# Kernel tuning notes

Measured on AMD Instinct MI355X. Metric: run time of the kernel, lower is better.

The kernel has to match this reference:

```python
import jax, jax.numpy as jnp
import numpy as np

STATE_DIM = 512
PROJ_DIM = 300


def setup_inputs() -> dict:
    key = jax.random.key(0)
    ks = jax.random.split(key, 10)
    batseq, node_num, edge_num = 320, 32, 1024  # edge_num = node_num**2
    inp = {
        "nodes_feats": jax.random.normal(ks[0], (batseq, node_num, STATE_DIM), jnp.float32),
        "edges_feats": jax.random.normal(ks[1], (batseq, edge_num, STATE_DIM), jnp.float32),
        "adj_mat": jax.random.uniform(ks[2], (batseq, node_num, edge_num), jnp.float32),
        "true_lengths": jax.random.randint(ks[3], (32,), 0, 10),
        "seq_size": 10,
        # Linear layer params (out_features=300, in_features=512), torch layout W: [out, in]
        "W1": jax.random.normal(ks[4], (PROJ_DIM, STATE_DIM), jnp.float32) * 0.02,
        "b1": jnp.zeros((PROJ_DIM,), jnp.float32),
        "W2": jax.random.normal(ks[5], (PROJ_DIM, STATE_DIM), jnp.float32) * 0.02,
        "b2": jnp.zeros((PROJ_DIM,), jnp.float32),
        "W3": jax.random.normal(ks[6], (PROJ_DIM, STATE_DIM), jnp.float32) * 0.02,
        "b3": jnp.zeros((PROJ_DIM,), jnp.float32),
    }
    return inp


def reference(nodes_feats, edges_feats, adj_mat, true_lengths, seq_size,
              W1, b1, W2, b2, W3, b3):
    batseq, node_num, _ = nodes_feats.shape
    batch = batseq // seq_size  # from adj_mat.view(-1, seq_size, node_num, edge_num)
    # Batched replacements for the per-pair tiny Linears
    f1 = jnp.einsum("bnd,pd->bnp", nodes_feats, W1) + b1   # [B, N, 300]
    f3 = jnp.einsum("bnd,pd->bnp", nodes_feats, W3) + b3   # [B, N, 300]
    f2 = jnp.einsum("bed,pd->bep", edges_feats, W2) + b2   # [B, N*N, 300]
    f2 = f2.reshape(batseq, node_num, node_num, PROJ_DIM)  # [B, i, j, 300]
    # per-pair MSE(f_j, f_ij + f_i), mean over (batseq, 300), summed over (i, j)
    diff = f3[:, None, :, :] - f2 - f1[:, :, None, :]
    losses = jnp.sum(diff * diff) / (batseq * PROJ_DIM)
    return losses / batch
```

## Files before the change

kernel.cpp:

```cpp
#include <hip/hip_runtime.h>
#include <hip/hip_bf16.h>
#include <stdint.h>

#define STATE 512
#define PROJ 300
#define PPAD 320
#define BATSEQ 320
#define TE 327680
#define PSTR 328

typedef __bf16 bf16x8 __attribute__((ext_vector_type(8)));
typedef float f32x4 __attribute__((ext_vector_type(4)));
typedef float f32x2 __attribute__((ext_vector_type(2)));
typedef long long i64;

__device__ inline unsigned short f2bf(float x) {
  unsigned u = __builtin_bit_cast(unsigned, x);
  unsigned r = u + 0x7fffu + ((u >> 16) & 1u);
  return (unsigned short)(r >> 16);
}

__global__ __launch_bounds__(256) void prep_kernel(
    const float* __restrict__ W1, const float* __restrict__ b1,
    const float* __restrict__ W2, const float* __restrict__ b2,
    const float* __restrict__ W3, const float* __restrict__ b3,
    unsigned short* __restrict__ w1p, unsigned short* __restrict__ w3p,
    unsigned short* __restrict__ w2tp, unsigned char* __restrict__ w2p8,
    float* __restrict__ b1p, float* __restrict__ b2p, float* __restrict__ b3p)
{
  int idx = blockIdx.x * 256 + threadIdx.x;
  const int WN = PPAD * STATE;
  if (idx < 2 * WN) {
    int which = idx / WN, r = idx % WN;
    int cs = r / 512, q = r % 512;
    int lane = q / 8, i = q % 8;
    int c = cs / 16, s = cs % 16;
    int p = c * 16 + (lane & 15);
    int k = s * 32 + (lane >> 4) * 8 + i;
    const float* W = (which == 0) ? W1 : W3;
    unsigned short* dst = (which == 0) ? w1p : w3p;
    float v = (p < PROJ) ? W[(size_t)p * STATE + k] : 0.0f;
    dst[r] = f2bf(v);
  } else if (idx < 3 * WN) {
    int r = idx - 2 * WN;
    int cs = r / 512, q = r % 512;
    int lane = q / 8, ii = q % 8;
    int ct = cs / 10, s2 = cs % 10;
    int p = s2 * 32 + (lane >> 4) * 8 + ii;
    int n = ct * 16 + (lane & 15);
    float v = (p < PROJ) ? W2[(size_t)p * STATE + n] : 0.0f;
    w2tp[r] = f2bf(v);
  } else if (idx < 4 * WN) {
    int r = idx - 3 * WN;
    int cs = r / 512, q = r % 512;
    int lane = q / 8, i = q % 8;
    int c = cs / 16, s = cs % 16;
    int p = c * 16 + (lane & 15);
    int k = s * 32 + (lane >> 4) * 8 + i;
    float v = (p < PROJ) ? W2[(size_t)p * STATE + k] : 0.0f;
    int pk = __builtin_amdgcn_cvt_pk_fp8_f32(v, 0.f, 0, 0);
    w2p8[r] = (unsigned char)(pk & 0xff);
  } else if (idx < 4 * WN + 3 * PPAD) {
    int r = idx - 4 * WN;
    int which = r / PPAD, p = r % PPAD;
    const float* B = (which == 0) ? b1 : ((which == 1) ? b2 : b3);
    float* dst = (which == 0) ? b1p : ((which == 1) ? b2p : b3p);
    dst[p] = (p < PROJ) ? B[p] : 0.0f;
  }
}

__global__ __launch_bounds__(256, 2) void node_kernel(
    const float* __restrict__ nodes,
    const unsigned short* __restrict__ w1p, const unsigned short* __restrict__ w3p,
    const unsigned short* __restrict__ w2tp,
    const float* __restrict__ b1p, const float* __restrict__ b2p,
    const float* __restrict__ b3p,
    float* __restrict__ g1t, float* __restrict__ g3t,
    double* __restrict__ pnode)
{
  __shared__ __align__(16) unsigned short tile[32 * 512];
  __shared__ __align__(16) unsigned short t2a[32 * PSTR];
  __shared__ __align__(16) unsigned short t2b[32 * PSTR];
  __shared__ float G1[PPAD], G3[PPAD];
  __shared__ double red[4];
  const int tid = threadIdx.x;
  const int wave = tid >> 6, lane = tid & 63;
  const int b = blockIdx.x;
  const float* src = nodes + (size_t)b * 32 * STATE;

  for (int t = tid; t < PPAD; t += 256) { G1[t] = 0.f; G3[t] = 0.f; }

  #pragma unroll
  for (int m = 0; m < 16; ++m) {
    int k = wave + 4 * m;
    int row = k >> 1;
    int fc = (k & 1) * 64 + lane;
    f32x4 v = *(const f32x4*)(src + row * STATE + fc * 4);
    unsigned lo = f2bf(v.x) | ((unsigned)f2bf(v.y) << 16);
    unsigned hi = f2bf(v.z) | ((unsigned)f2bf(v.w) << 16);
    unsigned long long pk = (unsigned long long)lo | ((unsigned long long)hi << 32);
    unsigned off = (unsigned)(row * 1024 + fc * 8) ^ (unsigned)((row & 7) << 4);
    *(unsigned long long*)((char*)tile + off) = pk;
  }
  __syncthreads();

  const int lrow = lane & 15, lk = lane >> 4;
  const int cbase = wave * 5;

  f32x4 af1[2][5], af3[2][5];
  #pragma unroll
  for (int rg = 0; rg < 2; ++rg)
    #pragma unroll
    for (int c = 0; c < 5; ++c) {
      af1[rg][c][0]=0.f; af1[rg][c][1]=0.f; af1[rg][c][2]=0.f; af1[rg][c][3]=0.f;
      af3[rg][c][0]=0.f; af3[rg][c][1]=0.f; af3[rg][c][2]=0.f; af3[rg][c][3]=0.f;
    }
  for (int s = 0; s < 16; ++s) {
    bf16x8 a[2];
    #pragma unroll
    for (int rg = 0; rg < 2; ++rg) {
      int row = rg * 16 + lrow;
      unsigned off = (unsigned)(row * 1024 + s * 64 + lk * 16) ^ (unsigned)((row & 7) << 4);
      a[rg] = *(const bf16x8*)((const char*)tile + off);
    }
    #pragma unroll
    for (int c = 0; c < 5; ++c) {
      size_t fo = ((size_t)(((cbase + c) * 16 + s) * 64 + lane)) * 8;
      bf16x8 bf1 = *(const bf16x8*)(w1p + fo);
      bf16x8 bf3 = *(const bf16x8*)(w3p + fo);
      #pragma unroll
      for (int rg = 0; rg < 2; ++rg) {
        af1[rg][c] = __builtin_amdgcn_mfma_f32_16x16x32_bf16(a[rg], bf1, af1[rg][c], 0, 0, 0);
        af3[rg][c] = __builtin_amdgcn_mfma_f32_16x16x32_bf16(a[rg], bf3, af3[rg][c], 0, 0, 0);
      }
    }
  }

  float sq = 0.f;
  #pragma unroll
  for (int rg = 0; rg < 2; ++rg)
    #pragma unroll
    for (int c = 0; c < 5; ++c) {
      int p = (cbase + c) * 16 + lrow;
      float bb1 = b1p[p], bb2 = b2p[p], bb3 = b3p[p];
      #pragma unroll
      for (int r = 0; r < 4; ++r) {
        int m = rg * 16 + lk * 4 + r;
        float v1 = af1[rg][c][r] + bb1;
        float v3 = af3[rg][c][r] + bb3 - bb2;
        t2a[m * PSTR + p] = f2bf(v1);
        t2b[m * PSTR + p] = f2bf(v3);
        sq += v1 * v1 + v3 * v3;
        atomicAdd(&G1[p], v1);
        atomicAdd(&G3[p], v3);
      }
    }
  __syncthreads();

  float s7 = 0.f;
  for (int t = tid; t < PPAD; t += 256) s7 += G3[t] * G1[t];
  float val = 32.f * sq - 2.f * s7;
  #pragma unroll
  for (int m = 32; m >= 1; m >>= 1) val += __shfl_xor(val, m, 64);
  if (lane == 0) red[wave] = (double)val;

  for (int pass = 0; pass < 2; ++pass) {
    const unsigned short* t2 = pass ? t2b : t2a;
    float* gt = pass ? g3t : g1t;
    f32x4 acc2[2][8];
    #pragma unroll
    for (int rg = 0; rg < 2; ++rg)
      #pragma unroll
      for (int cc = 0; cc < 8; ++cc) { acc2[rg][cc][0]=0.f; acc2[rg][cc][1]=0.f; acc2[rg][cc][2]=0.f; acc2[rg][cc][3]=0.f; }
    for (int s2 = 0; s2 < 10; ++s2) {
      bf16x8 a[2];
      #pragma unroll
      for (int rg = 0; rg < 2; ++rg) {
        int mrow = rg * 16 + lrow;
        a[rg] = *(const bf16x8*)(t2 + mrow * PSTR + s2 * 32 + lk * 8);
      }
      #pragma unroll
      for (int cc = 0; cc < 8; ++cc) {
        int ct = wave * 8 + cc;
        bf16x8 bfr = *(const bf16x8*)(w2tp + ((size_t)((ct * 10 + s2) * 64 + lane)) * 8);
        #pragma unroll
        for (int rg = 0; rg < 2; ++rg)
          acc2[rg][cc] = __builtin_amdgcn_mfma_f32_16x16x32_bf16(a[rg], bfr, acc2[rg][cc], 0, 0, 0);
      }
    }
    #pragma unroll
    for (int rg = 0; rg < 2; ++rg)
      #pragma unroll
      for (int cc = 0; cc < 8; ++cc) {
        int n = (wave * 8 + cc) * 16 + lrow;
        #pragma unroll
        for (int r = 0; r < 4; ++r) {
          int mm = rg * 16 + lk * 4 + r;
          gt[((size_t)b * 32 + mm) * STATE + n] = acc2[rg][cc][r];
        }
      }
  }

  __syncthreads();
  if (tid == 0) pnode[b] = red[0] + red[1] + red[2] + red[3];
}

__global__ __launch_bounds__(256, 3) void edge_kernel(
    const float* __restrict__ edges, const unsigned char* __restrict__ w2p8,
    const float* __restrict__ g1t, const float* __restrict__ g3t,
    double* __restrict__ pedge)
{
  __shared__ __align__(16) unsigned char tile[64 * 512];
  __shared__ double redd[4][2];
  const int tid = threadIdx.x;
  const int wave = tid >> 6, lane = tid & 63;

  const int orig = blockIdx.x;
  const int wg = (orig & 7) * 640 + (orig >> 3);
  const int b = wg >> 4, q = wg & 15;
  const float* src = edges + ((size_t)b * 1024 + (size_t)q * 64) * STATE;
  const float* g3b = g3t + (size_t)b * 32 * STATE;
  const float* g1b = g1t + ((size_t)b * 32 + (size_t)q * 2) * STATE;

  float cr = 0.f;
  f32x4 sE0 = {0.f, 0.f, 0.f, 0.f}, sE1 = {0.f, 0.f, 0.f, 0.f};
  const int fc = tid & 127;
  const int rhi = tid >> 7;
  #pragma unroll 16
  for (int m = 0; m < 32; ++m) {
    int row = 2 * m + rhi;
    f32x4 e = *(const f32x4*)(src + row * STATE + fc * 4);
    if (m < 16) sE0 += e; else sE1 += e;
    int pk = __builtin_amdgcn_cvt_pk_fp8_f32(e.x, e.y, 0, 0);
    pk = __builtin_amdgcn_cvt_pk_fp8_f32(e.z, e.w, pk, 1);
    unsigned off = (unsigned)(row * 512 + fc * 4) ^ (unsigned)((row & 7) << 3);
    *(int*)(tile + off) = pk;
  }
  {
    f32x4 g1a = *(const f32x4*)(g1b + fc * 4);
    f32x4 g1c = *(const f32x4*)(g1b + STATE + fc * 4);
    cr -= sE0.x * g1a.x + sE0.y * g1a.y + sE0.z * g1a.z + sE0.w * g1a.w;
    cr -= sE1.x * g1c.x + sE1.y * g1c.y + sE1.z * g1c.z + sE1.w * g1c.w;
  }
  __syncthreads();

  const int lrow = lane & 15, lk = lane >> 4;
  const int cb = wave * 5;
  f32x4 acc[4][5];
  #pragma unroll
  for (int rg = 0; rg < 4; ++rg)
    #pragma unroll
    for (int c = 0; c < 5; ++c) { acc[rg][c][0]=0.f; acc[rg][c][1]=0.f; acc[rg][c][2]=0.f; acc[rg][c][3]=0.f; }
  for (int s = 0; s < 16; ++s) {
    i64 a[4];
    #pragma unroll
    for (int rg = 0; rg < 4; ++rg) {
      int row = rg * 16 + lrow;
      unsigned off = (unsigned)(row * 512 + s * 32 + lk * 8) ^ (unsigned)((row & 7) << 3);
      a[rg] = *(const i64*)(tile + off);
    }
    #pragma unroll
    for (int c = 0; c < 5; ++c) {
      i64 bfr = *(const i64*)(w2p8 + ((size_t)(((cb + c) * 16 + s) * 64 + lane)) * 8);
      #pragma unroll
      for (int rg = 0; rg < 4; ++rg)
        acc[rg][c] = __builtin_amdgcn_mfma_f32_16x16x32_fp8_fp8(a[rg], bfr, acc[rg][c], 0, 0, 0);
    }
  }

  float ss = 0.f;
  #pragma unroll
  for (int rg = 0; rg < 4; ++rg)
    #pragma unroll
    for (int c = 0; c < 5; ++c)
      #pragma unroll
      for (int r = 0; r < 4; ++r) ss += acc[rg][c][r] * acc[rg][c][r];

  {
    const int j = tid >> 3, s8 = tid & 7;
    const float* g3r = g3b + (size_t)j * STATE + s8 * 64;
    const unsigned sw = (unsigned)((j & 7) << 3);
    float part = 0.f;
    #pragma unroll
    for (int c = 0; c < 8; ++c) {
      unsigned o0 = (unsigned)(j * 512 + s8 * 64 + c * 8) ^ sw;
      unsigned o1 = (unsigned)((j + 32) * 512 + s8 * 64 + c * 8) ^ sw;
      i64 p0 = *(const i64*)(tile + o0);
      i64 p1 = *(const i64*)(tile + o1);
      int l0 = (int)(p0 & 0xffffffffll), h0 = (int)(((unsigned long long)p0) >> 32);
      int l1 = (int)(p1 & 0xffffffffll), h1 = (int)(((unsigned long long)p1) >> 32);
      f32x2 a0 = __builtin_amdgcn_cvt_pk_f32_fp8(l0, 0);
      f32x2 a1 = __builtin_amdgcn_cvt_pk_f32_fp8(l0, 1);
      f32x2 a2 = __builtin_amdgcn_cvt_pk_f32_fp8(h0, 0);
      f32x2 a3 = __builtin_amdgcn_cvt_pk_f32_fp8(h0, 1);
      f32x2 c0 = __builtin_amdgcn_cvt_pk_f32_fp8(l1, 0);
      f32x2 c1 = __builtin_amdgcn_cvt_pk_f32_fp8(l1, 1);
      f32x2 c2 = __builtin_amdgcn_cvt_pk_f32_fp8(h1, 0);
      f32x2 c3 = __builtin_amdgcn_cvt_pk_f32_fp8(h1, 1);
      f32x4 g0 = *(const f32x4*)(g3r + c * 8);
      f32x4 g1v = *(const f32x4*)(g3r + c * 8 + 4);
      part += (a0.x + c0.x) * g0.x + (a0.y + c0.y) * g0.y
            + (a1.x + c1.x) * g0.z + (a1.y + c1.y) * g0.w
            + (a2.x + c2.x) * g1v.x + (a2.y + c2.y) * g1v.y
            + (a3.x + c3.x) * g1v.z + (a3.y + c3.y) * g1v.w;
    }
    cr += part;
  }

  #pragma unroll
  for (int m = 32; m >= 1; m >>= 1) {
    ss += __shfl_xor(ss, m, 64);
    cr += __shfl_xor(cr, m, 64);
  }
  if (lane == 0) { redd[wave][0] = (double)ss; redd[wave][1] = (double)cr; }
  __syncthreads();
  if (tid == 0) {
    double sT = 0.0, cT = 0.0;
    #pragma unroll
    for (int w = 0; w < 4; ++w) { sT += redd[w][0]; cT += redd[w][1]; }
    pedge[wg] = sT - 2.0 * cT;
  }
}

__global__ __launch_bounds__(256) void final_kernel(
    const double* __restrict__ pedge, const double* __restrict__ pnode,
    const int* __restrict__ seqp, float* __restrict__ out)
{
  __shared__ double red[4];
  const int tid = threadIdx.x, wave = tid >> 6, lane = tid & 63;
  double v = 0.0;
  for (int t = tid; t < 5120; t += 256) v += pedge[t];
  for (int t = tid; t < 320; t += 256) v += pnode[t];
  #pragma unroll
  for (int m = 32; m >= 1; m >>= 1) v += __shfl_xor(v, m, 64);
  if (lane == 0) red[wave] = v;
  __syncthreads();
  if (tid == 0) {
    double Total = red[0] + red[1] + red[2] + red[3];
    int seq = seqp[0];
    int batch = (seq > 0) ? (BATSEQ / seq) : 1;
    out[0] = (float)(Total / ((double)BATSEQ * (double)PROJ) / (double)batch);
  }
}

extern "C" void kernel_launch(void* const* d_in, const int* in_sizes, int n_in,
                              void* d_out, int out_size, void* d_ws, size_t ws_size,
                              hipStream_t stream)
{
  const float* nodes = (const float*)d_in[0];
  const float* edges = (const float*)d_in[1];
  const int*   seqp  = (const int*)d_in[4];
  const float* W1 = (const float*)d_in[5];
  const float* b1 = (const float*)d_in[6];
  const float* W2 = (const float*)d_in[7];
  const float* b2 = (const float*)d_in[8];
  const float* W3 = (const float*)d_in[9];
  const float* b3 = (const float*)d_in[10];

  char* ws = (char*)d_ws;
  unsigned short* w1p  = (unsigned short*)(ws + 0);
  unsigned short* w3p  = (unsigned short*)(ws + 327680);
  unsigned short* w2tp = (unsigned short*)(ws + 655360);
  unsigned char*  w2p8 = (unsigned char*)(ws + 983040);
  float* b1p = (float*)(ws + 1146880);
  float* b2p = (float*)(ws + 1148160);
  float* b3p = (float*)(ws + 1149440);
  float* g1t = (float*)(ws + 2097152);
  float* g3t = (float*)(ws + 23068672);
  double* pedge = (double*)(ws + 44040192);
  double* pnode = (double*)(ws + 44081152);

  prep_kernel<<<2564, 256, 0, stream>>>(W1, b1, W2, b2, W3, b3,
                                        w1p, w3p, w2tp, w2p8, b1p, b2p, b3p);
  node_kernel<<<320, 256, 0, stream>>>(nodes, w1p, w3p, w2tp, b1p, b2p, b3p,
                                       g1t, g3t, pnode);
  edge_kernel<<<5120, 256, 0, stream>>>(edges, w2p8, g1t, g3t, pedge);
  final_kernel<<<1, 256, 0, stream>>>(pedge, pnode, seqp, (float*)d_out);
}
```

Baseline: 309.4 us.

## Double edge tile per block and compute g3 cross term with fp8 MFMA

Each edge block now handles 128 edge rows instead of 64, halving the grid and reusing each W2 fragment load across twice as many MFMAs. The scalar fp8-to-float dot product against g3 is replaced by extra MFMAs against a g3 matrix pre-packed to fp8 by a new small kernel, with only the diagonal entries kept. This trades higher register and LDS use, and lower occupancy (launch bounds drop to 2 blocks), for fewer global weight reads and less scalar ALU work. The g3 term now also runs at fp8 precision.

```diff
diff --git a/kernel.cpp b/kernel.cpp
--- a/kernel.cpp
+++ b/kernel.cpp
@@ -11,7 +11,6 @@
 
 typedef __bf16 bf16x8 __attribute__((ext_vector_type(8)));
 typedef float f32x4 __attribute__((ext_vector_type(4)));
-typedef float f32x2 __attribute__((ext_vector_type(2)));
 typedef long long i64;
 
 __device__ inline unsigned short f2bf(float x) {
@@ -205,106 +204,118 @@
   if (tid == 0) pnode[b] = red[0] + red[1] + red[2] + red[3];
 }
 
-__global__ __launch_bounds__(256, 3) void edge_kernel(
+__global__ __launch_bounds__(256) void g3pack_kernel(
+    const float* __restrict__ g3t, unsigned char* __restrict__ g3p8)
+{
+  const int b = blockIdx.x;
+  const float* g3b = g3t + (size_t)b * 32 * STATE;
+  int* dst = (int*)(g3p8 + (size_t)b * 16384);
+  #pragma unroll
+  for (int t = 0; t < 16; ++t) {
+    int g = threadIdx.x + t * 256;
+    int r = g * 4;
+    int lane = (r >> 3) & 63;
+    int i0 = r & 7;
+    int cts = r >> 9;
+    int j = (cts >> 4) * 16 + (lane & 15);
+    int k = (cts & 15) * 32 + (lane >> 4) * 8 + i0;
+    const float* v = g3b + (size_t)j * STATE + k;
+    int pk = __builtin_amdgcn_cvt_pk_fp8_f32(v[0], v[1], 0, 0);
+    pk = __builtin_amdgcn_cvt_pk_fp8_f32(v[2], v[3], pk, 1);
+    dst[g] = pk;
+  }
+}
+
+__global__ __launch_bounds__(256, 2) void edge_kernel(
     const float* __restrict__ edges, const unsigned char* __restrict__ w2p8,
-    const float* __restrict__ g1t, const float* __restrict__ g3t,
+    const unsigned char* __restrict__ g3p8, const float* __restrict__ g1t,
     double* __restrict__ pedge)
 {
-  __shared__ __align__(16) unsigned char tile[64 * 512];
+  __shared__ __align__(16) unsigned char tile[128 * 512];
   __shared__ double redd[4][2];
   const int tid = threadIdx.x;
   const int wave = tid >> 6, lane = tid & 63;
 
   const int orig = blockIdx.x;
-  const int wg = (orig & 7) * 640 + (orig >> 3);
-  const int b = wg >> 4, q = wg & 15;
-  const float* src = edges + ((size_t)b * 1024 + (size_t)q * 64) * STATE;
-  const float* g3b = g3t + (size_t)b * 32 * STATE;
-  const float* g1b = g1t + ((size_t)b * 32 + (size_t)q * 2) * STATE;
-
-  float cr = 0.f;
-  f32x4 sE0 = {0.f, 0.f, 0.f, 0.f}, sE1 = {0.f, 0.f, 0.f, 0.f};
+  const int wg = (orig & 7) * 320 + (orig >> 3);
+  const int b = wg >> 3, q4 = wg & 7;
+  const float* src = edges + ((size_t)b * 1024 + (size_t)q4 * 128) * STATE;
+  const unsigned char* g3p = g3p8 + (size_t)b * 16384;
+  const float* g1b = g1t + ((size_t)b * 32 + (size_t)q4 * 4) * STATE;
+
+  f32x4 sE[4];
+  #pragma unroll
+  for (int ii = 0; ii < 4; ++ii) { sE[ii][0]=0.f; sE[ii][1]=0.f; sE[ii][2]=0.f; sE[ii][3]=0.f; }
   const int fc = tid & 127;
   const int rhi = tid >> 7;
   #pragma unroll 16
-  for (int m = 0; m < 32; ++m) {
+  for (int m = 0; m < 64; ++m) {
     int row = 2 * m + rhi;
     f32x4 e = *(const f32x4*)(src + row * STATE + fc * 4);
-    if (m < 16) sE0 += e; else sE1 += e;
+    sE[m >> 4] += e;
     int pk = __builtin_amdgcn_cvt_pk_fp8_f32(e.x, e.y, 0, 0);
     pk = __builtin_amdgcn_cvt_pk_fp8_f32(e.z, e.w, pk, 1);
     unsigned off = (unsigned)(row * 512 + fc * 4) ^ (unsigned)((row & 7) << 3);
     *(int*)(tile + off) = pk;
   }
-  {
-    f32x4 g1a = *(const f32x4*)(g1b + fc * 4);
-    f32x4 g1c = *(const f32x4*)(g1b + STATE + fc * 4);
-    cr -= sE0.x * g1a.x + sE0.y * g1a.y + sE0.z * g1a.z + sE0.w * g1a.w;
-    cr -= sE1.x * g1c.x + sE1.y * g1c.y + sE1.z * g1c.z + sE1.w * g1c.w;
-  }
   __syncthreads();
 
   const int lrow = lane & 15, lk = lane >> 4;
   const int cb = wave * 5;
-  f32x4 acc[4][5];
-  #pragma unroll
-  for (int rg = 0; rg < 4; ++rg)
+  f32x4 acc[8][5];
+  #pragma unroll
+  for (int rg = 0; rg < 8; ++rg)
     #pragma unroll
     for (int c = 0; c < 5; ++c) { acc[rg][c][0]=0.f; acc[rg][c][1]=0.f; acc[rg][c][2]=0.f; acc[rg][c][3]=0.f; }
+  f32x4 accg[2];
+  accg[0][0]=0.f; accg[0][1]=0.f; accg[0][2]=0.f; accg[0][3]=0.f;
+  accg[1][0]=0.f; accg[1][1]=0.f; accg[1][2]=0.f; accg[1][3]=0.f;
+
+  #pragma unroll 4
   for (int s = 0; s < 16; ++s) {
-    i64 a[4];
-    #pragma unroll
-    for (int rg = 0; rg < 4; ++rg) {
+    i64 a[8];
+    #pragma unroll
+    for (int rg = 0; rg < 8; ++rg) {
       int row = rg * 16 + lrow;
-      unsigned off = (unsigned)(row * 512 + s * 32 + lk * 8) ^ (unsigned)((row & 7) << 3);
+      unsigned off = (unsigned)(row * 512 + s * 32 + lk * 8) ^ (unsigned)((lrow & 7) << 3);
       a[rg] = *(const i64*)(tile + off);
     }
+    i64 bg0 = *(const i64*)(g3p + ((size_t)((s) * 64 + lane)) * 8);
+    i64 bg1 = *(const i64*)(g3p + ((size_t)((16 + s) * 64 + lane)) * 8);
     #pragma unroll
     for (int c = 0; c < 5; ++c) {
       i64 bfr = *(const i64*)(w2p8 + ((size_t)(((cb + c) * 16 + s) * 64 + lane)) * 8);
       #pragma unroll
-      for (int rg = 0; rg < 4; ++rg)
+      for (int rg = 0; rg < 8; ++rg)
         acc[rg][c] = __builtin_amdgcn_mfma_f32_16x16x32_fp8_fp8(a[rg], bfr, acc[rg][c], 0, 0, 0);
     }
-  }
-
-  float ss = 0.f;
-  #pragma unroll
-  for (int rg = 0; rg < 4; ++rg)
+    #pragma unroll
+    for (int rg = 0; rg < 8; ++rg)
+      accg[rg & 1] = __builtin_amdgcn_mfma_f32_16x16x32_fp8_fp8(a[rg], (rg & 1) ? bg1 : bg0, accg[rg & 1], 0, 0, 0);
+  }
+
+  float ss = 0.f, cr = 0.f;
+  #pragma unroll
+  for (int rg = 0; rg < 8; ++rg)
     #pragma unroll
     for (int c = 0; c < 5; ++c)
       #pragma unroll
       for (int r = 0; r < 4; ++r) ss += acc[rg][c][r] * acc[rg][c][r];
 
   {
-    const int j = tid >> 3, s8 = tid & 7;
-    const float* g3r = g3b + (size_t)j * STATE + s8 * 64;
-    const unsigned sw = (unsigned)((j & 7) << 3);
-    float part = 0.f;
-    #pragma unroll
-    for (int c = 0; c < 8; ++c) {
-      unsigned o0 = (unsigned)(j * 512 + s8 * 64 + c * 8) ^ sw;
-      unsigned o1 = (unsigned)((j + 32) * 512 + s8 * 64 + c * 8) ^ sw;
-      i64 p0 = *(const i64*)(tile + o0);
-      i64 p1 = *(const i64*)(tile + o1);
-      int l0 = (int)(p0 & 0xffffffffll), h0 = (int)(((unsigned long long)p0) >> 32);
-      int l1 = (int)(p1 & 0xffffffffll), h1 = (int)(((unsigned long long)p1) >> 32);
-      f32x2 a0 = __builtin_amdgcn_cvt_pk_f32_fp8(l0, 0);
-      f32x2 a1 = __builtin_amdgcn_cvt_pk_f32_fp8(l0, 1);
-      f32x2 a2 = __builtin_amdgcn_cvt_pk_f32_fp8(h0, 0);
-      f32x2 a3 = __builtin_amdgcn_cvt_pk_f32_fp8(h0, 1);
-      f32x2 c0 = __builtin_amdgcn_cvt_pk_f32_fp8(l1, 0);
-      f32x2 c1 = __builtin_amdgcn_cvt_pk_f32_fp8(l1, 1);
-      f32x2 c2 = __builtin_amdgcn_cvt_pk_f32_fp8(h1, 0);
-      f32x2 c3 = __builtin_amdgcn_cvt_pk_f32_fp8(h1, 1);
-      f32x4 g0 = *(const f32x4*)(g3r + c * 8);
-      f32x4 g1v = *(const f32x4*)(g3r + c * 8 + 4);
-      part += (a0.x + c0.x) * g0.x + (a0.y + c0.y) * g0.y
-            + (a1.x + c1.x) * g0.z + (a1.y + c1.y) * g0.w
-            + (a2.x + c2.x) * g1v.x + (a2.y + c2.y) * g1v.y
-            + (a3.x + c3.x) * g1v.z + (a3.y + c3.y) * g1v.w;
-    }
-    cr += part;
+    int qv = lane & 15, hi4 = lane >> 4;
+    if ((qv >> 2) == hi4) {
+      int r = qv & 3;
+      float d0 = (r == 0) ? accg[0][0] : (r == 1) ? accg[0][1] : (r == 2) ? accg[0][2] : accg[0][3];
+      float d1 = (r == 0) ? accg[1][0] : (r == 1) ? accg[1][1] : (r == 2) ? accg[1][2] : accg[1][3];
+      cr += d0 + d1;
+    }
+  }
+
+  #pragma unroll
+  for (int ii = 0; ii < 4; ++ii) {
+    f32x4 g1v = *(const f32x4*)(g1b + (size_t)ii * STATE + fc * 4);
+    cr -= sE[ii].x * g1v.x + sE[ii].y * g1v.y + sE[ii].z * g1v.z + sE[ii].w * g1v.w;
   }
 
   #pragma unroll
@@ -329,7 +340,7 @@
   __shared__ double red[4];
   const int tid = threadIdx.x, wave = tid >> 6, lane = tid & 63;
   double v = 0.0;
-  for (int t = tid; t < 5120; t += 256) v += pedge[t];
+  for (int t = tid; t < 2560; t += 256) v += pedge[t];
   for (int t = tid; t < 320; t += 256) v += pnode[t];
   #pragma unroll
   for (int m = 32; m >= 1; m >>= 1) v += __shfl_xor(v, m, 64);
@@ -368,12 +379,14 @@
   float* g1t = (float*)(ws + 2097152);
   float* g3t = (float*)(ws + 23068672);
   double* pedge = (double*)(ws + 44040192);
-  double* pnode = (double*)(ws + 44081152);
+  double* pnode = (double*)(ws + 44060672);
+  unsigned char* g3p8 = (unsigned char*)(ws + 44072960);
 
   prep_kernel<<<2564, 256, 0, stream>>>(W1, b1, W2, b2, W3, b3,
                                         w1p, w3p, w2tp, w2p8, b1p, b2p, b3p);
   node_kernel<<<320, 256, 0, stream>>>(nodes, w1p, w3p, w2tp, b1p, b2p, b3p,
                                        g1t, g3t, pnode);
-  edge_kernel<<<5120, 256, 0, stream>>>(edges, w2p8, g1t, g3t, pedge);
+  g3pack_kernel<<<320, 256, 0, stream>>>(g3t, g3p8);
+  edge_kernel<<<2560, 256, 0, stream>>>(edges, w2p8, g3p8, g1t, pedge);
   final_kernel<<<1, 256, 0, stream>>>(pedge, pnode, seqp, (float*)d_out);
 }
```

Result: slower. 347.6 us (+12.3%).

## Split edge kernel into FP8 compress pass and LDS-direct MFMA pass

Applied to the files above, without the earlier changes.

Moves the fp32-to-fp8 conversion of edge features and the cross-term dot products into a separate compress kernel that writes swizzled fp8 tiles to global workspace. The edge kernel then loads these tiles straight into LDS with global_load_lds and runs only the MFMA sum-of-squares. The cross term now uses the full-precision fp32 edges instead of the dequantized fp8 values. This adds an extra global write and read of about 168 MB of fp8 data plus a kernel launch, in exchange for simpler kernels that may reach better occupancy or overlap.

```diff
diff --git a/kernel.cpp b/kernel.cpp
--- a/kernel.cpp
+++ b/kernel.cpp
@@ -11,7 +11,6 @@
 
 typedef __bf16 bf16x8 __attribute__((ext_vector_type(8)));
 typedef float f32x4 __attribute__((ext_vector_type(4)));
-typedef float f32x2 __attribute__((ext_vector_type(2)));
 typedef long long i64;
 
 __device__ inline unsigned short f2bf(float x) {
@@ -205,13 +204,12 @@
   if (tid == 0) pnode[b] = red[0] + red[1] + red[2] + red[3];
 }
 
-__global__ __launch_bounds__(256, 3) void edge_kernel(
-    const float* __restrict__ edges, const unsigned char* __restrict__ w2p8,
-    const float* __restrict__ g1t, const float* __restrict__ g3t,
-    double* __restrict__ pedge)
-{
-  __shared__ __align__(16) unsigned char tile[64 * 512];
-  __shared__ double redd[4][2];
+__global__ __launch_bounds__(256) void compress_kernel(
+    const float* __restrict__ edges, const float* __restrict__ g1t,
+    const float* __restrict__ g3t, unsigned char* __restrict__ e8g,
+    double* __restrict__ pcross)
+{
+  __shared__ double redd[4];
   const int tid = threadIdx.x;
   const int wave = tid >> 6, lane = tid & 63;
 
@@ -219,6 +217,7 @@
   const int wg = (orig & 7) * 640 + (orig >> 3);
   const int b = wg >> 4, q = wg & 15;
   const float* src = edges + ((size_t)b * 1024 + (size_t)q * 64) * STATE;
+  unsigned char* dst = e8g + (size_t)wg * 32768;
   const float* g3b = g3t + (size_t)b * 32 * STATE;
   const float* g1b = g1t + ((size_t)b * 32 + (size_t)q * 2) * STATE;
 
@@ -226,15 +225,17 @@
   f32x4 sE0 = {0.f, 0.f, 0.f, 0.f}, sE1 = {0.f, 0.f, 0.f, 0.f};
   const int fc = tid & 127;
   const int rhi = tid >> 7;
-  #pragma unroll 16
+  #pragma unroll 8
   for (int m = 0; m < 32; ++m) {
     int row = 2 * m + rhi;
-    f32x4 e = *(const f32x4*)(src + row * STATE + fc * 4);
+    f32x4 e  = *(const f32x4*)(src + row * STATE + fc * 4);
+    f32x4 g3 = *(const f32x4*)(g3b + (row & 31) * STATE + fc * 4);
+    cr += e.x * g3.x + e.y * g3.y + e.z * g3.z + e.w * g3.w;
     if (m < 16) sE0 += e; else sE1 += e;
     int pk = __builtin_amdgcn_cvt_pk_fp8_f32(e.x, e.y, 0, 0);
     pk = __builtin_amdgcn_cvt_pk_fp8_f32(e.z, e.w, pk, 1);
     unsigned off = (unsigned)(row * 512 + fc * 4) ^ (unsigned)((row & 7) << 3);
-    *(int*)(tile + off) = pk;
+    *(int*)(dst + off) = pk;
   }
   {
     f32x4 g1a = *(const f32x4*)(g1b + fc * 4);
@@ -242,6 +243,37 @@
     cr -= sE0.x * g1a.x + sE0.y * g1a.y + sE0.z * g1a.z + sE0.w * g1a.w;
     cr -= sE1.x * g1c.x + sE1.y * g1c.y + sE1.z * g1c.z + sE1.w * g1c.w;
   }
+
+  #pragma unroll
+  for (int m = 32; m >= 1; m >>= 1) cr += __shfl_xor(cr, m, 64);
+  if (lane == 0) redd[wave] = (double)cr;
+  __syncthreads();
+  if (tid == 0) pcross[wg] = redd[0] + redd[1] + redd[2] + redd[3];
+}
+
+__global__ __launch_bounds__(256, 3) void edge_kernel(
+    const unsigned char* __restrict__ e8g, const unsigned char* __restrict__ w2p8,
+    double* __restrict__ pedge)
+{
+  __shared__ __align__(16) unsigned char tile[64 * 512];
+  __shared__ double redd[4];
+  const int tid = threadIdx.x;
+  const int wave = tid >> 6, lane = tid & 63;
+
+  const int orig = blockIdx.x;
+  const int wg = (orig & 7) * 640 + (orig >> 3);
+  const unsigned char* srcp = e8g + (size_t)wg * 32768;
+
+  {
+    char* ldsw = (char*)tile + wave * 8192;
+    #pragma unroll
+    for (int t = 0; t < 8; ++t) {
+      __builtin_amdgcn_global_load_lds(
+          (const __attribute__((address_space(1))) unsigned int*)(srcp + wave * 8192 + t * 1024 + lane * 16),
+          (__attribute__((address_space(3))) unsigned int*)(ldsw + t * 1024),
+          16, 0, 0);
+    }
+  }
   __syncthreads();
 
   const int lrow = lane & 15, lk = lane >> 4;
@@ -276,60 +308,22 @@
       #pragma unroll
       for (int r = 0; r < 4; ++r) ss += acc[rg][c][r] * acc[rg][c][r];
 
-  {
-    const int j = tid >> 3, s8 = tid & 7;
-    const float* g3r = g3b + (size_t)j * STATE + s8 * 64;
-    const unsigned sw = (unsigned)((j & 7) << 3);
-    float part = 0.f;
-    #pragma unroll
-    for (int c = 0; c < 8; ++c) {
-      unsigned o0 = (unsigned)(j * 512 + s8 * 64 + c * 8) ^ sw;
-      unsigned o1 = (unsigned)((j + 32) * 512 + s8 * 64 + c * 8) ^ sw;
-      i64 p0 = *(const i64*)(tile + o0);
-      i64 p1 = *(const i64*)(tile + o1);
-      int l0 = (int)(p0 & 0xffffffffll), h0 = (int)(((unsigned long long)p0) >> 32);
-      int l1 = (int)(p1 & 0xffffffffll), h1 = (int)(((unsigned long long)p1) >> 32);
-      f32x2 a0 = __builtin_amdgcn_cvt_pk_f32_fp8(l0, 0);
-      f32x2 a1 = __builtin_amdgcn_cvt_pk_f32_fp8(l0, 1);
-      f32x2 a2 = __builtin_amdgcn_cvt_pk_f32_fp8(h0, 0);
-      f32x2 a3 = __builtin_amdgcn_cvt_pk_f32_fp8(h0, 1);
-      f32x2 c0 = __builtin_amdgcn_cvt_pk_f32_fp8(l1, 0);
-      f32x2 c1 = __builtin_amdgcn_cvt_pk_f32_fp8(l1, 1);
-      f32x2 c2 = __builtin_amdgcn_cvt_pk_f32_fp8(h1, 0);
-      f32x2 c3 = __builtin_amdgcn_cvt_pk_f32_fp8(h1, 1);
-      f32x4 g0 = *(const f32x4*)(g3r + c * 8);
-      f32x4 g1v = *(const f32x4*)(g3r + c * 8 + 4);
-      part += (a0.x + c0.x) * g0.x + (a0.y + c0.y) * g0.y
-            + (a1.x + c1.x) * g0.z + (a1.y + c1.y) * g0.w
-            + (a2.x + c2.x) * g1v.x + (a2.y + c2.y) * g1v.y
-            + (a3.x + c3.x) * g1v.z + (a3.y + c3.y) * g1v.w;
-    }
-    cr += part;
-  }
-
-  #pragma unroll
-  for (int m = 32; m >= 1; m >>= 1) {
-    ss += __shfl_xor(ss, m, 64);
-    cr += __shfl_xor(cr, m, 64);
-  }
-  if (lane == 0) { redd[wave][0] = (double)ss; redd[wave][1] = (double)cr; }
-  __syncthreads();
-  if (tid == 0) {
-    double sT = 0.0, cT = 0.0;
-    #pragma unroll
-    for (int w = 0; w < 4; ++w) { sT += redd[w][0]; cT += redd[w][1]; }
-    pedge[wg] = sT - 2.0 * cT;
-  }
+  #pragma unroll
+  for (int m = 32; m >= 1; m >>= 1) ss += __shfl_xor(ss, m, 64);
+  if (lane == 0) redd[wave] = (double)ss;
+  __syncthreads();
+  if (tid == 0) pedge[wg] = redd[0] + redd[1] + redd[2] + redd[3];
 }
 
 __global__ __launch_bounds__(256) void final_kernel(
-    const double* __restrict__ pedge, const double* __restrict__ pnode,
-    const int* __restrict__ seqp, float* __restrict__ out)
+    const double* __restrict__ pedge, const double* __restrict__ pcross,
+    const double* __restrict__ pnode, const int* __restrict__ seqp,
+    float* __restrict__ out)
 {
   __shared__ double red[4];
   const int tid = threadIdx.x, wave = tid >> 6, lane = tid & 63;
   double v = 0.0;
-  for (int t = tid; t < 5120; t += 256) v += pedge[t];
+  for (int t = tid; t < 5120; t += 256) v += pedge[t] - 2.0 * pcross[t];
   for (int t = tid; t < 320; t += 256) v += pnode[t];
   #pragma unroll
   for (int m = 32; m >= 1; m >>= 1) v += __shfl_xor(v, m, 64);
@@ -367,13 +361,16 @@
   float* b3p = (float*)(ws + 1149440);
   float* g1t = (float*)(ws + 2097152);
   float* g3t = (float*)(ws + 23068672);
-  double* pedge = (double*)(ws + 44040192);
-  double* pnode = (double*)(ws + 44081152);
+  double* pedge  = (double*)(ws + 44040192);
+  double* pcross = (double*)(ws + 44081152);
+  double* pnode  = (double*)(ws + 44122112);
+  unsigned char* e8g = (unsigned char*)(ws + 46137344);
 
   prep_kernel<<<2564, 256, 0, stream>>>(W1, b1, W2, b2, W3, b3,
                                         w1p, w3p, w2tp, w2p8, b1p, b2p, b3p);
   node_kernel<<<320, 256, 0, stream>>>(nodes, w1p, w3p, w2tp, b1p, b2p, b3p,
                                        g1t, g3t, pnode);
-  edge_kernel<<<5120, 256, 0, stream>>>(edges, w2p8, g1t, g3t, pedge);
-  final_kernel<<<1, 256, 0, stream>>>(pedge, pnode, seqp, (float*)d_out);
-}
+  compress_kernel<<<5120, 256, 0, stream>>>(edges, g1t, g3t, e8g, pcross);
+  edge_kernel<<<5120, 256, 0, stream>>>(e8g, w2p8, pedge);
+  final_kernel<<<1, 256, 0, stream>>>(pedge, pcross, pnode, seqp, (float*)d_out);
+}
```

New measurement: 391.9 us. 1.27x slower.
